# Kernel tuning notes

Measured on AMD Instinct MI355X. Metric: run time of the kernel, lower is better.

Reference implementation:

```python
import jax, jax.numpy as jnp
import numpy as np

BS, N_CTX, N_HEADS, WIDTH = 2, 2048, 8, 32
N_TOK = 512


def setup_inputs() -> dict:
    key = jax.random.key(0)
    kq, kk, kv, ki = jax.random.split(key, 4)
    q = jax.random.normal(kq, (BS, N_CTX, N_HEADS, WIDTH), dtype=jnp.float32)
    k = jax.random.normal(kk, (BS, N_CTX, N_HEADS, WIDTH), dtype=jnp.float32)
    v = jax.random.normal(kv, (BS, N_CTX, N_HEADS, WIDTH), dtype=jnp.float32)
    indx = jnp.sort(jax.random.randint(ki, (N_TOK,), 0, N_CTX, dtype=jnp.int64))
    return {"q": q, "k": k, "v": v, "indx": indx}


def reference(q, k, v, indx):
    # q, k, v: (bs, n_ctx, n_heads, width); indx: (n_tok,) token ids to attend over
    n_tok = indx.shape[0]
    scale = jnp.float32(1.0 / np.sqrt(n_tok))
    qg = q[:, indx]  # (bs, n_tok, h, w) -- gathered tokens (t axis in torch code)
    kg = k[:, indx]  # (bs, n_tok, h, w) -- gathered tokens (s axis in torch code)
    vg = v[:, indx]  # (bs, n_tok, h, w)
    # L1 distance scores: ww[b,s,t,h] = scale * sum_w |q[b,indx[t],h,w] - k[b,indx[s],h,w]|
    diff = jnp.abs(qg[:, None, :, :, :] - kg[:, :, None, :, :])  # (bs, s, t, h, w)
    scores = -scale * jnp.sum(diff, axis=-1)  # (bs, s, t, h)
    attn = jax.nn.softmax(scores, axis=2)  # softmax over t (matches torch softmax(-1) on (b,h,s,t))
    # out[b,s,h,w] = sum_t attn[b,s,t,h] * v[b,indx[t],h,w]
    out = jnp.einsum('bsth,bthw->bshw', attn, vg)
    return out
```

## Files before the change

kernel.cpp:

```cpp
#include <hip/hip_runtime.h>

#define NCTX 2048
#define NH   8
#define WD   32
#define NTOK 512

static constexpr float SCALE = 0.04419417382415922f;

typedef float f32x16 __attribute__((ext_vector_type(16)));

template<int JPW, bool PARTIAL>
__global__ __launch_bounds__(1024, 4) void l1attn_main(
    const float* __restrict__ q, const float* __restrict__ k,
    const float* __restrict__ v, const int* __restrict__ indx,
    float* __restrict__ dst ) {
  __shared__ int   indxS[NTOK];
  __shared__ float accS[64 * 33];
  __shared__ float lS[64];

  const int tid = threadIdx.x;
  if (tid < NTOK) indxS[tid] = indx[tid];
  for (int i = tid; i < 64 * 33; i += 1024) accS[i] = 0.f;
  if (tid < 64) lS[tid] = 0.f;
  __syncthreads();

  const int wave = __builtin_amdgcn_readfirstlane(tid >> 6);
  const int lane = tid & 63;

  int pr, jbase;
  if (PARTIAL) { pr = blockIdx.x >> 1; jbase = ((blockIdx.x & 1) * 16 + wave) * 16; }
  else         { pr = blockIdx.x;      jbase = wave * 32; }
  const int plane = pr >> 3;
  const int rg    = pr & 7;
  const int b     = plane >> 3;
  const int h     = plane & 7;

  const float* qb = q + ((size_t)b * NCTX * NH + h) * WD;
  const float* vb = v + ((size_t)b * NCTX * NH + h) * WD;
  const float* kb = k + ((size_t)b * NCTX * NH + h) * WD;

  float kg[32];
  {
    const int s = rg * 64 + lane;
    const float4* kr = (const float4*)(kb + (size_t)indxS[s] * (NH * WD));
#pragma unroll
    for (int i = 0; i < 8; ++i) {
      float4 t = kr[i];
      kg[4*i+0] = t.x; kg[4*i+1] = t.y; kg[4*i+2] = t.z; kg[4*i+3] = t.w;
    }
  }

  float acc[32];
#pragma unroll
  for (int i = 0; i < 32; ++i) acc[i] = 0.f;
  float l = 0.f;

  int tok = __builtin_amdgcn_readfirstlane(indxS[jbase]);
  for (int jj = 0; jj < JPW; ++jj) {
    const int tokn =
        __builtin_amdgcn_readfirstlane(indxS[jbase + ((jj + 1) & (JPW - 1))]);
    const float* qp = qb + (size_t)tok * (NH * WD);
    const float* vp = vb + (size_t)tok * (NH * WD);

    f32x16 q0, q1, v0, v1;
    asm volatile(
        "s_load_dwordx16 %0, %4, 0x0\n\t"
        "s_load_dwordx16 %1, %4, 0x40\n\t"
        "s_load_dwordx16 %2, %5, 0x0\n\t"
        "s_load_dwordx16 %3, %5, 0x40\n\t"
        "s_waitcnt lgkmcnt(0)"
        : "=&s"(q0), "=&s"(q1), "=&s"(v0), "=&s"(v1)
        : "s"(qp), "s"(vp));

    float d0, d1, d2, d3;
    d0 = fabsf(q0[0] - kg[0]);
    d1 = fabsf(q0[1] - kg[1]);
    d2 = fabsf(q0[2] - kg[2]);
    d3 = fabsf(q0[3] - kg[3]);
#pragma unroll
    for (int i = 1; i < 4; ++i) {
      d0 += fabsf(q0[4*i+0] - kg[4*i+0]);
      d1 += fabsf(q0[4*i+1] - kg[4*i+1]);
      d2 += fabsf(q0[4*i+2] - kg[4*i+2]);
      d3 += fabsf(q0[4*i+3] - kg[4*i+3]);
    }
#pragma unroll
    for (int i = 0; i < 4; ++i) {
      d0 += fabsf(q1[4*i+0] - kg[16+4*i+0]);
      d1 += fabsf(q1[4*i+1] - kg[16+4*i+1]);
      d2 += fabsf(q1[4*i+2] - kg[16+4*i+2]);
      d3 += fabsf(q1[4*i+3] - kg[16+4*i+3]);
    }
    const float d = (d0 + d1) + (d2 + d3);
    const float p = __expf(-SCALE * d);
    l += p;
#pragma unroll
    for (int i = 0; i < 16; ++i) {
      acc[i]      = fmaf(p, v0[i], acc[i]);
      acc[16 + i] = fmaf(p, v1[i], acc[16 + i]);
    }
    tok = tokn;
  }

#pragma unroll
  for (int w = 0; w < 32; ++w) atomicAdd(&accS[lane * 33 + w], acc[w]);
  atomicAdd(&lS[lane], l);
  __syncthreads();

  if (PARTIAL) {
    float* wsB = dst + (size_t)blockIdx.x * 2176;
    for (int i = tid; i < 64 * 33; i += 1024) wsB[i] = accS[i];
    if (tid < 64) wsB[64 * 33 + tid] = lS[tid];
  } else {
#pragma unroll
    for (int idx = tid; idx < 2048; idx += 1024) {
      const int r = idx >> 5, w = idx & 31;
      dst[(((size_t)b * NTOK + rg * 64 + r) * NH + h) * WD + w] =
          accS[r * 33 + w] / lS[r];
    }
  }
}

__global__ __launch_bounds__(1024) void l1attn_combine(
    const float* __restrict__ ws, float* __restrict__ out) {
  const int gid = blockIdx.x * 1024 + threadIdx.x;
  const int w  = gid & 31;
  const int r  = (gid >> 5) & 63;
  const int pr = gid >> 11;
  const int b  = pr >> 6, h = (pr >> 3) & 7, rg = pr & 7;
  const float* pa = ws + (size_t)(2 * pr)     * 2176;
  const float* pb = ws + (size_t)(2 * pr + 1) * 2176;
  const float acc = pa[r * 33 + w] + pb[r * 33 + w];
  const float lsum = pa[2112 + r] + pb[2112 + r];
  out[(((size_t)b * NTOK + rg * 64 + r) * NH + h) * WD + w] = acc / lsum;
}

extern "C" void kernel_launch(void* const* d_in, const int* in_sizes, int n_in,
                              void* d_out, int out_size, void* d_ws, size_t ws_size,
                              hipStream_t stream) {
  const float* q    = (const float*)d_in[0];
  const float* k    = (const float*)d_in[1];
  const float* v    = (const float*)d_in[2];
  const int*   indx = (const int*)d_in[3];
  float*       out  = (float*)d_out;

  const size_t need = (size_t)256 * 2176 * sizeof(float);
  if (ws_size >= need) {
    hipLaunchKernelGGL((l1attn_main<16, true>), dim3(256), dim3(1024), 0, stream,
                       q, k, v, indx, (float*)d_ws);
    hipLaunchKernelGGL(l1attn_combine, dim3(256), dim3(1024), 0, stream,
                       (const float*)d_ws, out);
  } else {
    hipLaunchKernelGGL((l1attn_main<32, false>), dim3(128), dim3(1024), 0, stream,
                       q, k, v, indx, out);
  }
}
```

Measured before the change: 60.36 us.

## Stage gathered Q/V rows in LDS and split key dimension four ways

Each block now cooperatively gathers a window of Q and V rows into shared memory and reads them from LDS, replacing the per-wave scalar s_load of every token's rows. Blocks shrink to 512 threads, and the token range is split across 4 blocks per row group (512 blocks in total), with a templated combine kernel that sums S partials. The aim is to drop the scalar-load latency stall on each iteration and to raise parallelism. The cost is more LDS traffic per iteration, an extra barrier, and a larger workspace for the partials.

New measurement: 66.09 us. 1.09x slower.

```diff
diff --git a/kernel.cpp b/kernel.cpp
--- a/kernel.cpp
+++ b/kernel.cpp
@@ -7,38 +7,46 @@
 
 static constexpr float SCALE = 0.04419417382415922f;
 
-typedef float f32x16 __attribute__((ext_vector_type(16)));
-
-template<int JPW, bool PARTIAL>
-__global__ __launch_bounds__(1024, 4) void l1attn_main(
+template<int S>
+__global__ __launch_bounds__(512, 4) void l1attn_main(
     const float* __restrict__ q, const float* __restrict__ k,
     const float* __restrict__ v, const int* __restrict__ indx,
     float* __restrict__ dst ) {
+  constexpr int WIN = NTOK / S;
   __shared__ int   indxS[NTOK];
+  __shared__ float ldsQ[WIN * 32];
+  __shared__ float ldsV[WIN * 32];
   __shared__ float accS[64 * 33];
   __shared__ float lS[64];
 
-  const int tid = threadIdx.x;
-  if (tid < NTOK) indxS[tid] = indx[tid];
-  for (int i = tid; i < 64 * 33; i += 1024) accS[i] = 0.f;
+  const int tid  = threadIdx.x;
+  const int bid  = blockIdx.x;
+  const int pr   = bid / S;
+  const int jw   = bid % S;
+  const int b    = pr >> 6;
+  const int h    = (pr >> 3) & 7;
+  const int rg   = pr & 7;
+
+  indxS[tid] = indx[tid];
+  for (int i = tid; i < 64 * 33; i += 512) accS[i] = 0.f;
   if (tid < 64) lS[tid] = 0.f;
   __syncthreads();
 
+  const float* qb = q + ((size_t)b * NCTX * NH) * WD + h * WD;
+  const float* vb = v + ((size_t)b * NCTX * NH) * WD + h * WD;
+  const float* kb = k + ((size_t)b * NCTX * NH) * WD + h * WD;
+
+  for (int i = tid; i < WIN * 8; i += 512) {
+    const int t = i >> 3, sg = i & 7;
+    const int tok = indxS[jw * WIN + t];
+    const float4* qr = (const float4*)(qb + (size_t)tok * (NH * WD));
+    const float4* vr = (const float4*)(vb + (size_t)tok * (NH * WD));
+    ((float4*)ldsQ)[i] = qr[sg];
+    ((float4*)ldsV)[i] = vr[sg];
+  }
+
+  const int lane = tid & 63;
   const int wave = __builtin_amdgcn_readfirstlane(tid >> 6);
-  const int lane = tid & 63;
-
-  int pr, jbase;
-  if (PARTIAL) { pr = blockIdx.x >> 1; jbase = ((blockIdx.x & 1) * 16 + wave) * 16; }
-  else         { pr = blockIdx.x;      jbase = wave * 32; }
-  const int plane = pr >> 3;
-  const int rg    = pr & 7;
-  const int b     = plane >> 3;
-  const int h     = plane & 7;
-
-  const float* qb = q + ((size_t)b * NCTX * NH + h) * WD;
-  const float* vb = v + ((size_t)b * NCTX * NH + h) * WD;
-  const float* kb = k + ((size_t)b * NCTX * NH + h) * WD;
-
   float kg[32];
   {
     const int s = rg * 64 + lane;
@@ -55,51 +63,39 @@
   for (int i = 0; i < 32; ++i) acc[i] = 0.f;
   float l = 0.f;
 
-  int tok = __builtin_amdgcn_readfirstlane(indxS[jbase]);
+  __syncthreads();
+
+  constexpr int JPW = WIN / 8;
+  const int jloc0 = wave * JPW;
   for (int jj = 0; jj < JPW; ++jj) {
-    const int tokn =
-        __builtin_amdgcn_readfirstlane(indxS[jbase + ((jj + 1) & (JPW - 1))]);
-    const float* qp = qb + (size_t)tok * (NH * WD);
-    const float* vp = vb + (size_t)tok * (NH * WD);
-
-    f32x16 q0, q1, v0, v1;
-    asm volatile(
-        "s_load_dwordx16 %0, %4, 0x0\n\t"
-        "s_load_dwordx16 %1, %4, 0x40\n\t"
-        "s_load_dwordx16 %2, %5, 0x0\n\t"
-        "s_load_dwordx16 %3, %5, 0x40\n\t"
-        "s_waitcnt lgkmcnt(0)"
-        : "=&s"(q0), "=&s"(q1), "=&s"(v0), "=&s"(v1)
-        : "s"(qp), "s"(vp));
+    const float* qrow = ldsQ + (jloc0 + jj) * 32;
+    const float* vrow = ldsV + (jloc0 + jj) * 32;
 
     float d0, d1, d2, d3;
-    d0 = fabsf(q0[0] - kg[0]);
-    d1 = fabsf(q0[1] - kg[1]);
-    d2 = fabsf(q0[2] - kg[2]);
-    d3 = fabsf(q0[3] - kg[3]);
-#pragma unroll
-    for (int i = 1; i < 4; ++i) {
-      d0 += fabsf(q0[4*i+0] - kg[4*i+0]);
-      d1 += fabsf(q0[4*i+1] - kg[4*i+1]);
-      d2 += fabsf(q0[4*i+2] - kg[4*i+2]);
-      d3 += fabsf(q0[4*i+3] - kg[4*i+3]);
+    {
+      float4 t = ((const float4*)qrow)[0];
+      d0 = fabsf(t.x - kg[0]); d1 = fabsf(t.y - kg[1]);
+      d2 = fabsf(t.z - kg[2]); d3 = fabsf(t.w - kg[3]);
     }
 #pragma unroll
-    for (int i = 0; i < 4; ++i) {
-      d0 += fabsf(q1[4*i+0] - kg[16+4*i+0]);
-      d1 += fabsf(q1[4*i+1] - kg[16+4*i+1]);
-      d2 += fabsf(q1[4*i+2] - kg[16+4*i+2]);
-      d3 += fabsf(q1[4*i+3] - kg[16+4*i+3]);
+    for (int i = 1; i < 8; ++i) {
+      float4 t = ((const float4*)qrow)[i];
+      d0 += fabsf(t.x - kg[4*i+0]);
+      d1 += fabsf(t.y - kg[4*i+1]);
+      d2 += fabsf(t.z - kg[4*i+2]);
+      d3 += fabsf(t.w - kg[4*i+3]);
     }
     const float d = (d0 + d1) + (d2 + d3);
     const float p = __expf(-SCALE * d);
     l += p;
 #pragma unroll
-    for (int i = 0; i < 16; ++i) {
-      acc[i]      = fmaf(p, v0[i], acc[i]);
-      acc[16 + i] = fmaf(p, v1[i], acc[16 + i]);
+    for (int i = 0; i < 8; ++i) {
+      float4 t = ((const float4*)vrow)[i];
+      acc[4*i+0] = fmaf(p, t.x, acc[4*i+0]);
+      acc[4*i+1] = fmaf(p, t.y, acc[4*i+1]);
+      acc[4*i+2] = fmaf(p, t.z, acc[4*i+2]);
+      acc[4*i+3] = fmaf(p, t.w, acc[4*i+3]);
     }
-    tok = tokn;
   }
 
 #pragma unroll
@@ -107,32 +103,36 @@
   atomicAdd(&lS[lane], l);
   __syncthreads();
 
-  if (PARTIAL) {
-    float* wsB = dst + (size_t)blockIdx.x * 2176;
-    for (int i = tid; i < 64 * 33; i += 1024) wsB[i] = accS[i];
-    if (tid < 64) wsB[64 * 33 + tid] = lS[tid];
+  if (S > 1) {
+    float* wsB = dst + (size_t)bid * 2112;
+    for (int i = tid; i < 2048; i += 512)
+      wsB[i] = accS[(i >> 5) * 33 + (i & 31)];
+    if (tid < 64) wsB[2048 + tid] = lS[tid];
   } else {
-#pragma unroll
-    for (int idx = tid; idx < 2048; idx += 1024) {
-      const int r = idx >> 5, w = idx & 31;
+    for (int i = tid; i < 2048; i += 512) {
+      const int r = i >> 5, w = i & 31;
       dst[(((size_t)b * NTOK + rg * 64 + r) * NH + h) * WD + w] =
           accS[r * 33 + w] / lS[r];
     }
   }
 }
 
+template<int S>
 __global__ __launch_bounds__(1024) void l1attn_combine(
     const float* __restrict__ ws, float* __restrict__ out) {
   const int gid = blockIdx.x * 1024 + threadIdx.x;
   const int w  = gid & 31;
   const int r  = (gid >> 5) & 63;
   const int pr = gid >> 11;
-  const int b  = pr >> 6, h = (pr >> 3) & 7, rg = pr & 7;
-  const float* pa = ws + (size_t)(2 * pr)     * 2176;
-  const float* pb = ws + (size_t)(2 * pr + 1) * 2176;
-  const float acc = pa[r * 33 + w] + pb[r * 33 + w];
-  const float lsum = pa[2112 + r] + pb[2112 + r];
-  out[(((size_t)b * NTOK + rg * 64 + r) * NH + h) * WD + w] = acc / lsum;
+  const float* base = ws + (size_t)pr * S * 2112;
+  float a = 0.f, ls = 0.f;
+#pragma unroll
+  for (int jwi = 0; jwi < S; ++jwi) {
+    a  += base[jwi * 2112 + r * 32 + w];
+    ls += base[jwi * 2112 + 2048 + r];
+  }
+  const int b = pr >> 6, h = (pr >> 3) & 7, rg = pr & 7;
+  out[(((size_t)b * NTOK + rg * 64 + r) * NH + h) * WD + w] = a / ls;
 }
 
 extern "C" void kernel_launch(void* const* d_in, const int* in_sizes, int n_in,
@@ -144,14 +144,20 @@
   const int*   indx = (const int*)d_in[3];
   float*       out  = (float*)d_out;
 
-  const size_t need = (size_t)256 * 2176 * sizeof(float);
-  if (ws_size >= need) {
-    hipLaunchKernelGGL((l1attn_main<16, true>), dim3(256), dim3(1024), 0, stream,
+  const size_t need4 = (size_t)512 * 2112 * sizeof(float);
+  const size_t need2 = (size_t)256 * 2112 * sizeof(float);
+  if (ws_size >= need4) {
+    hipLaunchKernelGGL((l1attn_main<4>), dim3(512), dim3(512), 0, stream,
                        q, k, v, indx, (float*)d_ws);
-    hipLaunchKernelGGL(l1attn_combine, dim3(256), dim3(1024), 0, stream,
+    hipLaunchKernelGGL((l1attn_combine<4>), dim3(256), dim3(1024), 0, stream,
+                       (const float*)d_ws, out);
+  } else if (ws_size >= need2) {
+    hipLaunchKernelGGL((l1attn_main<2>), dim3(256), dim3(512), 0, stream,
+                       q, k, v, indx, (float*)d_ws);
+    hipLaunchKernelGGL((l1attn_combine<2>), dim3(256), dim3(1024), 0, stream,
                        (const float*)d_ws, out);
   } else {
-    hipLaunchKernelGGL((l1attn_main<32, false>), dim3(128), dim3(1024), 0, stream,
+    hipLaunchKernelGGL((l1attn_main<1>), dim3(128), dim3(512), 0, stream,
                        q, k, v, indx, out);
   }
 }
```
